# Optimization experiments

Measured on AMD Instinct MI355X. Metric: run time of the kernel, lower is better.

## Reference

```python
import jax, jax.numpy as jnp
import numpy as np

LN_EPS = 1e-5


def _layer_norm(x, w, b, eps=LN_EPS):
    mu = jnp.mean(x, axis=-1, keepdims=True)
    var = jnp.var(x, axis=-1, keepdims=True)
    return (x - mu) * jax.lax.rsqrt(var + eps) * w + b


def setup_inputs() -> dict:
    key = jax.random.key(0)
    ks = jax.random.split(key, 6)
    H, I, B, S = 1024, 4096, 4, 2048
    return {
        "x": jax.random.normal(ks[0], (B, S, H), jnp.float32),
        "ln_weight": jnp.ones((H,), jnp.float32),
        "ln_bias": jnp.zeros((H,), jnp.float32),
        "i2h_weight": jax.random.normal(ks[1], (2 * I, H), jnp.float32) * 0.02,
        "i2h_bias": jax.random.normal(ks[2], (2 * I,), jnp.float32) * 0.02,
        "h2o_weight": jax.random.normal(ks[3], (H, I), jnp.float32) * 0.02,
        "h2o_bias": jax.random.normal(ks[4], (H,), jnp.float32) * 0.02,
        "post_ln_weight": jnp.ones((H,), jnp.float32),
        "post_ln_bias": jnp.zeros((H,), jnp.float32),
    }


def reference(x, ln_weight, ln_bias, i2h_weight, i2h_bias, h2o_weight, h2o_bias,
              post_ln_weight, post_ln_bias):
    B, S, H = x.shape
    x2 = x.reshape(-1, H)  # [N, H]
    x_ln = _layer_norm(x2, ln_weight, ln_bias)
    # i2h: [N, 2I]
    pre = jnp.einsum('nh,oh->no', x_ln, i2h_weight) + i2h_bias
    I = pre.shape[-1] // 2
    pre_gate, lin = pre[:, :I], pre[:, I:]
    # gated gelu (tanh-approx, matching gelu_fused)
    hid = jax.nn.gelu(pre_gate, approximate=True) * lin
    out = jnp.einsum('ni,oi->no', hid, h2o_weight) + h2o_bias
    out = _layer_norm(out, post_ln_weight, post_ln_bias)
    out = out + x2  # residual (dropout=0)
    return out.reshape(B, S, H)
```

## Files before the change

### kernel.cpp

```cpp
#include <hip/hip_runtime.h>
#include <stdint.h>

#define N_ROWS 8192
#define H_DIM  1024
#define I_DIM  4096

typedef unsigned short u16;
typedef __bf16 bf16x8 __attribute__((ext_vector_type(8)));
typedef float f32x4 __attribute__((ext_vector_type(4)));
typedef u16 u16x4 __attribute__((ext_vector_type(4)));

#define BAR()   asm volatile("s_barrier" ::: "memory")
#define VMW(n)  asm volatile("s_waitcnt vmcnt(" #n ")" ::: "memory")

__device__ __forceinline__ u16 f2bf(float f) {
    union { float f; uint32_t u; } v; v.f = f;
    uint32_t u = v.u;
    u += 0x7FFFu + ((u >> 16) & 1u);
    return (u16)(u >> 16);
}

__device__ __forceinline__ float bf2f(u16 h) {
    union { uint32_t u; float f; } v; v.u = ((uint32_t)h) << 16;
    return v.f;
}

__device__ __forceinline__ float gelu_tanh(float x) {
    float u = 0.7978845608028654f * (x + 0.044715f * x * x * x);
    u = fminf(fmaxf(u, -15.f), 15.f);
    float e = __expf(2.f * u);
    float t = (e - 1.f) / (e + 1.f);
    return 0.5f * x * (1.f + t);
}

__device__ __forceinline__ void load_lds16(const void* g, void* l) {
    auto gp = reinterpret_cast<const __attribute__((address_space(1))) uint32_t*>(
        reinterpret_cast<uintptr_t>(g));
    auto lp = reinterpret_cast<__attribute__((address_space(3))) uint32_t*>(
        static_cast<uint32_t>(reinterpret_cast<uintptr_t>(l)));
    __builtin_amdgcn_global_load_lds(gp, lp, 16, 0, 0);
}

__global__ __launch_bounds__(512, 2) void gemm1_gated(
    const u16* __restrict__ A, const u16* __restrict__ W,
    const float* __restrict__ bias, u16* __restrict__ hid)
{
    __shared__ u16 lds[3 * 16384];
    const int t = threadIdx.x;
    const int lane = t & 63, wid = t >> 6;
    const int wm = wid >> 2, wn = wid & 3;
    const int g = lane >> 4, r16 = lane & 15;

    const int brow = blockIdx.y * 256;
    const int bcol = blockIdx.x * 128;

    const int tr = t >> 2;
    const int swz8 = ((t & 3) ^ ((tr >> 1) & 3)) * 8;
    const u16* pA = A + (size_t)(brow + tr) * H_DIM + swz8;
    const int j0 = tr, j1 = tr + 128;
    const int c0 = bcol + ((j0 >> 6) << 5) + (j0 & 31);
    const int c1 = bcol + ((j1 >> 6) << 5) + (j1 & 31);
    const u16* pB0 = W + (size_t)(((j0 & 63) < 32) ? c0 : (I_DIM + c0)) * H_DIM + swz8;
    const u16* pB1 = W + (size_t)(((j1 & 63) < 32) ? c1 : (I_DIM + c1)) * H_DIM + swz8;
    const int dst = t * 8;

    const int sl  = (g ^ ((r16 >> 1) & 3)) * 8;
    const int rdA = (wm * 128 + r16) * 32 + sl;
    const int rdB = 8192 + (wn * 64 + r16) * 32 + sl;

    f32x4 acc[8][4] = {};

#define STG1(S, k0) do { \
    load_lds16(pA  + (k0),                       (S) + dst); \
    load_lds16(pA  + (size_t)128 * H_DIM + (k0), (S) + 4096 + dst); \
    load_lds16(pB0 + (k0),                       (S) + 8192 + dst); \
    load_lds16(pB1 + (k0),                       (S) + 12288 + dst); } while (0)

    STG1(lds, 0);
    STG1(lds + 16384, 32);
    VMW(4); BAR();

    const int NT = H_DIM / 32;
    int bc = 0;
#pragma unroll 1
    for (int kt = 0; kt < NT; ++kt) {
        const u16* L = lds + bc * 16384;
        const bool st = (kt + 2 < NT);
        if (st) {
            u16* S = lds + ((bc + 2 >= 3) ? (bc - 1) : (bc + 2)) * 16384;
            STG1(S, (kt + 2) * 32);
        }
        bf16x8 af[8], bf[4];
#pragma unroll
        for (int m = 0; m < 8; ++m) af[m] = *(const bf16x8*)(L + rdA + m * 512);
#pragma unroll
        for (int n = 0; n < 4; ++n) bf[n] = *(const bf16x8*)(L + rdB + n * 512);
        __builtin_amdgcn_s_setprio(1);
#pragma unroll
        for (int m = 0; m < 8; ++m)
#pragma unroll
            for (int n = 0; n < 4; ++n)
                acc[m][n] = __builtin_amdgcn_mfma_f32_16x16x32_bf16(af[m], bf[n], acc[m][n], 0, 0, 0);
        __builtin_amdgcn_s_setprio(0);
        if (st) { VMW(4); } else { VMW(0); }
        BAR();
        bc = (bc == 2) ? 0 : bc + 1;
    }
#undef STG1

#pragma unroll
    for (int n = 0; n < 2; ++n) {
        const int cg = bcol + wn * 32 + n * 16 + r16;
        const float bgv = bias[cg], blv = bias[I_DIM + cg];
#pragma unroll
        for (int m = 0; m < 8; ++m) {
            const int row = brow + wm * 128 + m * 16 + g * 4;
            u16* hp = hid + (size_t)row * I_DIM + cg;
#pragma unroll
            for (int r = 0; r < 4; ++r) {
                float gate = acc[m][n][r] + bgv;
                float lin  = acc[m][n + 2][r] + blv;
                hp[(size_t)r * I_DIM] = f2bf(gelu_tanh(gate) * lin);
            }
        }
    }
}

__global__ __launch_bounds__(256, 3) void gemm2_k(
    const u16* __restrict__ A, const u16* __restrict__ W,
    const float* __restrict__ bias, u16* __restrict__ opb)
{
    __shared__ u16 lds[3 * 8192];
    const int t = threadIdx.x;
    const int lane = t & 63, wid = t >> 6;
    const int wm = wid >> 1, wn = wid & 1;
    const int g = lane >> 4, r16 = lane & 15;

    const int brow = blockIdx.y * 128;
    const int bcol = blockIdx.x * 128;

    const int tr = t >> 2;
    const int swz8 = ((t & 3) ^ ((tr >> 1) & 3)) * 8;
    const u16* pA = A + (size_t)(brow + tr) * I_DIM + swz8;
    const u16* pB = W + (size_t)(bcol + tr) * I_DIM + swz8;
    const int dst = t * 8;

    const int sl  = (g ^ ((r16 >> 1) & 3)) * 8;
    const int rdA = (wm * 64 + r16) * 32 + sl;
    const int rdB = 4096 + (wn * 64 + r16) * 32 + sl;

    f32x4 acc[4][4] = {};

#define STG2(S, k0) do { \
    load_lds16(pA + (k0),                      (S) + dst); \
    load_lds16(pA + (size_t)64 * I_DIM + (k0), (S) + 2048 + dst); \
    load_lds16(pB + (k0),                      (S) + 4096 + dst); \
    load_lds16(pB + (size_t)64 * I_DIM + (k0), (S) + 6144 + dst); } while (0)

    STG2(lds, 0);
    STG2(lds + 8192, 32);
    VMW(4); BAR();

    const int NT = I_DIM / 32;
    int bc = 0;
#pragma unroll 1
    for (int kt = 0; kt < NT; ++kt) {
        const u16* L = lds + bc * 8192;
        if (kt + 2 < NT) {
            u16* S = lds + ((bc + 2 >= 3) ? (bc - 1) : (bc + 2)) * 8192;
            STG2(S, (kt + 2) * 32);
        }
        bf16x8 af[4], bf[4];
#pragma unroll
        for (int m = 0; m < 4; ++m) af[m] = *(const bf16x8*)(L + rdA + m * 512);
#pragma unroll
        for (int n = 0; n < 4; ++n) bf[n] = *(const bf16x8*)(L + rdB + n * 512);
        __builtin_amdgcn_s_setprio(1);
#pragma unroll
        for (int m = 0; m < 4; ++m)
#pragma unroll
            for (int n = 0; n < 4; ++n)
                acc[m][n] = __builtin_amdgcn_mfma_f32_16x16x32_bf16(af[m], bf[n], acc[m][n], 0, 0, 0);
        __builtin_amdgcn_s_setprio(0);
        if (kt + 2 < NT) { VMW(4); } else { VMW(0); }
        BAR();
        bc = (bc == 2) ? 0 : bc + 1;
    }
#undef STG2

#pragma unroll
    for (int n = 0; n < 4; ++n) {
        const int cg = bcol + wn * 64 + n * 16 + r16;
        const float bv = bias[cg];
#pragma unroll
        for (int m = 0; m < 4; ++m) {
            const int row = brow + wm * 64 + m * 16 + g * 4;
            u16* op = opb + (size_t)row * H_DIM + cg;
#pragma unroll
            for (int r = 0; r < 4; ++r)
                op[(size_t)r * H_DIM] = f2bf(acc[m][n][r] + bv);
        }
    }
}

__device__ __forceinline__ void block_mean_var(float s, float s2, float* red, int t,
                                               float& mu, float& var) {
#pragma unroll
    for (int off = 32; off > 0; off >>= 1) {
        s  += __shfl_down(s, off);
        s2 += __shfl_down(s2, off);
    }
    const int wid = t >> 6;
    if ((t & 63) == 0) { red[wid] = s; red[4 + wid] = s2; }
    __syncthreads();
    if (t == 0) {
        float a = red[0] + red[1] + red[2] + red[3];
        float b = red[4] + red[5] + red[6] + red[7];
        red[0] = a * (1.f / H_DIM);
        red[1] = b * (1.f / H_DIM);
    }
    __syncthreads();
    mu = red[0];
    var = red[1] - mu * mu;
}

__global__ __launch_bounds__(256) void prep(
    const float* __restrict__ x, const float* __restrict__ lnw,
    const float* __restrict__ lnb, u16* __restrict__ xln,
    const float* __restrict__ w1, u16* __restrict__ w1b,
    const float* __restrict__ w2, u16* __restrict__ w2b)
{
    __shared__ float red[8];
    const int bid = blockIdx.x, t = threadIdx.x;
    if (bid < N_ROWS) {
        const float4 v = reinterpret_cast<const float4*>(x + (size_t)bid * H_DIM)[t];
        float mu, var;
        block_mean_var(v.x + v.y + v.z + v.w,
                       v.x * v.x + v.y * v.y + v.z * v.z + v.w * v.w, red, t, mu, var);
        const float rstd = rsqrtf(var + 1e-5f);
        const float4 wv = reinterpret_cast<const float4*>(lnw)[t];
        const float4 bv = reinterpret_cast<const float4*>(lnb)[t];
        u16x4 o;
        o.x = f2bf((v.x - mu) * rstd * wv.x + bv.x);
        o.y = f2bf((v.y - mu) * rstd * wv.y + bv.y);
        o.z = f2bf((v.z - mu) * rstd * wv.z + bv.z);
        o.w = f2bf((v.w - mu) * rstd * wv.w + bv.w);
        reinterpret_cast<u16x4*>(xln + (size_t)bid * H_DIM)[t] = o;
    } else if (bid < N_ROWS + 8192) {
        const int i = (bid - N_ROWS) * 256 + t;
        const float4 v = reinterpret_cast<const float4*>(w1)[i];
        u16x4 o = { f2bf(v.x), f2bf(v.y), f2bf(v.z), f2bf(v.w) };
        reinterpret_cast<u16x4*>(w1b)[i] = o;
    } else {
        const int i = (bid - N_ROWS - 8192) * 256 + t;
        const float4 v = reinterpret_cast<const float4*>(w2)[i];
        u16x4 o = { f2bf(v.x), f2bf(v.y), f2bf(v.z), f2bf(v.w) };
        reinterpret_cast<u16x4*>(w2b)[i] = o;
    }
}

__global__ void ln_post_res(const u16* __restrict__ op, const float* __restrict__ w,
                            const float* __restrict__ b, const float* __restrict__ x,
                            float* __restrict__ out)
{
    __shared__ float red[8];
    const int row = blockIdx.x, t = threadIdx.x;
    const u16x4 hv = reinterpret_cast<const u16x4*>(op + (size_t)row * H_DIM)[t];
    float4 v;
    v.x = bf2f(hv.x); v.y = bf2f(hv.y); v.z = bf2f(hv.z); v.w = bf2f(hv.w);
    float mu, var;
    block_mean_var(v.x + v.y + v.z + v.w,
                   v.x * v.x + v.y * v.y + v.z * v.z + v.w * v.w, red, t, mu, var);
    const float rstd = rsqrtf(var + 1e-5f);
    const float4 wv = reinterpret_cast<const float4*>(w)[t];
    const float4 bv = reinterpret_cast<const float4*>(b)[t];
    const float4 xv = reinterpret_cast<const float4*>(x + (size_t)row * H_DIM)[t];
    float4 o;
    o.x = (v.x - mu) * rstd * wv.x + bv.x + xv.x;
    o.y = (v.y - mu) * rstd * wv.y + bv.y + xv.y;
    o.z = (v.z - mu) * rstd * wv.z + bv.z + xv.z;
    o.w = (v.w - mu) * rstd * wv.w + bv.w + xv.w;
    reinterpret_cast<float4*>(out + (size_t)row * H_DIM)[t] = o;
}

extern "C" void kernel_launch(void* const* d_in, const int* in_sizes, int n_in,
                              void* d_out, int out_size, void* d_ws, size_t ws_size,
                              hipStream_t stream)
{
    const float* x   = (const float*)d_in[0];
    const float* lnw = (const float*)d_in[1];
    const float* lnb = (const float*)d_in[2];
    const float* w1  = (const float*)d_in[3];
    const float* b1  = (const float*)d_in[4];
    const float* w2  = (const float*)d_in[5];
    const float* b2  = (const float*)d_in[6];
    const float* pw  = (const float*)d_in[7];
    const float* pb  = (const float*)d_in[8];
    float* out = (float*)d_out;

    char* ws = (char*)d_ws;
    u16* xln = (u16*)(ws);
    u16* w1b = (u16*)(ws + (16u << 20));
    u16* hid = (u16*)(ws + (32u << 20));
    u16* w2b = (u16*)(ws + (96u << 20));
    u16* opb = (u16*)(ws);

    prep<<<20480, 256, 0, stream>>>(x, lnw, lnb, xln, w1, w1b, w2, w2b);
    gemm1_gated<<<dim3(I_DIM / 128, N_ROWS / 256), 512, 0, stream>>>(xln, w1b, b1, hid);
    gemm2_k<<<dim3(H_DIM / 128, N_ROWS / 128), 256, 0, stream>>>(hid, w2b, b2, opb);
    ln_post_res<<<N_ROWS, 256, 0, stream>>>(opb, pw, pb, x, out);
}
```

Baseline: 274.9 us.

## Switch GEMMs to 32x32 MFMA with B operands loaded directly into registers

Both GEMM kernels move from 16x16x32 to 32x32x16 bf16 MFMA tiles. Each wave now loads its B (weight) fragments straight from global memory into registers, one k-step ahead, so only A is staged through LDS. The LDS swizzle changes to match the new read pattern. gemm2 grows to 256-row tiles with 512 threads. The goal is less LDS traffic and fewer LDS reads per MFMA, at the cost of uncoalesced per-wave global loads for B and higher register pressure.

Measured after the change: 416.7 us. 51.5% more time.

```diff
diff --git a/kernel.cpp b/kernel.cpp
--- a/kernel.cpp
+++ b/kernel.cpp
@@ -7,7 +7,7 @@
 
 typedef unsigned short u16;
 typedef __bf16 bf16x8 __attribute__((ext_vector_type(8)));
-typedef float f32x4 __attribute__((ext_vector_type(4)));
+typedef float f32x16 __attribute__((ext_vector_type(16)));
 typedef u16 u16x4 __attribute__((ext_vector_type(4)));
 
 #define BAR()   asm volatile("s_barrier" ::: "memory")
@@ -45,88 +45,99 @@
     const u16* __restrict__ A, const u16* __restrict__ W,
     const float* __restrict__ bias, u16* __restrict__ hid)
 {
-    __shared__ u16 lds[3 * 16384];
+    __shared__ u16 lds[3 * 8192];
     const int t = threadIdx.x;
     const int lane = t & 63, wid = t >> 6;
     const int wm = wid >> 2, wn = wid & 3;
-    const int g = lane >> 4, r16 = lane & 15;
+    const int cl = lane & 31, kh = lane >> 5;
 
     const int brow = blockIdx.y * 256;
     const int bcol = blockIdx.x * 128;
 
     const int tr = t >> 2;
-    const int swz8 = ((t & 3) ^ ((tr >> 1) & 3)) * 8;
+    const int sstg = ((tr >> 1) & 3) ^ ((tr >> 3) & 3);
+    const int swz8 = ((t & 3) ^ sstg) * 8;
     const u16* pA = A + (size_t)(brow + tr) * H_DIM + swz8;
-    const int j0 = tr, j1 = tr + 128;
-    const int c0 = bcol + ((j0 >> 6) << 5) + (j0 & 31);
-    const int c1 = bcol + ((j1 >> 6) << 5) + (j1 & 31);
-    const u16* pB0 = W + (size_t)(((j0 & 63) < 32) ? c0 : (I_DIM + c0)) * H_DIM + swz8;
-    const u16* pB1 = W + (size_t)(((j1 & 63) < 32) ? c1 : (I_DIM + c1)) * H_DIM + swz8;
     const int dst = t * 8;
 
-    const int sl  = (g ^ ((r16 >> 1) & 3)) * 8;
-    const int rdA = (wm * 128 + r16) * 32 + sl;
-    const int rdB = 8192 + (wn * 64 + r16) * 32 + sl;
-
-    f32x4 acc[8][4] = {};
-
-#define STG1(S, k0) do { \
-    load_lds16(pA  + (k0),                       (S) + dst); \
-    load_lds16(pA  + (size_t)128 * H_DIM + (k0), (S) + 4096 + dst); \
-    load_lds16(pB0 + (k0),                       (S) + 8192 + dst); \
-    load_lds16(pB1 + (k0),                       (S) + 12288 + dst); } while (0)
-
-    STG1(lds, 0);
-    STG1(lds + 16384, 32);
+    const int s  = ((cl >> 1) & 3) ^ ((cl >> 3) & 3);
+    const int p0 = ((0 + kh) ^ s) * 8;
+    const int p1 = ((2 + kh) ^ s) * 8;
+    const int rdA = (wm * 128 + cl) * 32;
+
+    const u16* pBg = W + (size_t)(bcol + wn * 32 + cl) * H_DIM + kh * 8;
+    const u16* pBl = W + (size_t)(I_DIM + bcol + wn * 32 + cl) * H_DIM + kh * 8;
+
+    f32x16 acc[4][2] = {};
+
+#define G1_STAGE(k0, bs) do { \
+    u16* S = lds + (bs) * 8192; \
+    load_lds16(pA + (k0),                       S + dst); \
+    load_lds16(pA + (size_t)128 * H_DIM + (k0), S + 4096 + dst); } while (0)
+#define G1_LOADB(k0, B) do { \
+    B[0] = *(const bf16x8*)(pBg + (k0));        \
+    B[1] = *(const bf16x8*)(pBg + (k0) + 16);   \
+    B[2] = *(const bf16x8*)(pBl + (k0));        \
+    B[3] = *(const bf16x8*)(pBl + (k0) + 16);   } while (0)
+#define G1_COMP(bcur, B) do { \
+    const u16* L = lds + (bcur) * 8192 + rdA; \
+    __builtin_amdgcn_s_setprio(1); \
+    _Pragma("unroll") for (int ks = 0; ks < 2; ++ks) { \
+        const int pk = ks ? p1 : p0; \
+        _Pragma("unroll") for (int tm = 0; tm < 4; ++tm) { \
+            bf16x8 af = *(const bf16x8*)(L + tm * 1024 + pk); \
+            acc[tm][0] = __builtin_amdgcn_mfma_f32_32x32x16_bf16(af, B[ks],     acc[tm][0], 0, 0, 0); \
+            acc[tm][1] = __builtin_amdgcn_mfma_f32_32x32x16_bf16(af, B[2 + ks], acc[tm][1], 0, 0, 0); \
+        } } \
+    __builtin_amdgcn_s_setprio(0); } while (0)
+
+    bf16x8 b0[4], b1[4];
+    G1_STAGE(0, 0);
+    G1_STAGE(32, 1);
+    __builtin_amdgcn_sched_barrier(0);
+    G1_LOADB(0, b0);
     VMW(4); BAR();
 
-    const int NT = H_DIM / 32;
     int bc = 0;
 #pragma unroll 1
-    for (int kt = 0; kt < NT; ++kt) {
-        const u16* L = lds + bc * 16384;
-        const bool st = (kt + 2 < NT);
-        if (st) {
-            u16* S = lds + ((bc + 2 >= 3) ? (bc - 1) : (bc + 2)) * 16384;
-            STG1(S, (kt + 2) * 32);
-        }
-        bf16x8 af[8], bf[4];
-#pragma unroll
-        for (int m = 0; m < 8; ++m) af[m] = *(const bf16x8*)(L + rdA + m * 512);
-#pragma unroll
-        for (int n = 0; n < 4; ++n) bf[n] = *(const bf16x8*)(L + rdB + n * 512);
-        __builtin_amdgcn_s_setprio(1);
-#pragma unroll
-        for (int m = 0; m < 8; ++m)
-#pragma unroll
-            for (int n = 0; n < 4; ++n)
-                acc[m][n] = __builtin_amdgcn_mfma_f32_16x16x32_bf16(af[m], bf[n], acc[m][n], 0, 0, 0);
-        __builtin_amdgcn_s_setprio(0);
-        if (st) { VMW(4); } else { VMW(0); }
+    for (int i = 0; i < 16; ++i) {
+        const bool w = (i < 15);
+        if (w) G1_STAGE((2 * i + 2) * 32, (bc + 2 >= 3) ? bc - 1 : bc + 2);
+        __builtin_amdgcn_sched_barrier(0);
+        G1_LOADB((2 * i + 1) * 32, b1);
+        G1_COMP(bc, b0);
+        if (w) { VMW(6); }
         BAR();
         bc = (bc == 2) ? 0 : bc + 1;
-    }
-#undef STG1
-
-#pragma unroll
-    for (int n = 0; n < 2; ++n) {
-        const int cg = bcol + wn * 32 + n * 16 + r16;
-        const float bgv = bias[cg], blv = bias[I_DIM + cg];
-#pragma unroll
-        for (int m = 0; m < 8; ++m) {
-            const int row = brow + wm * 128 + m * 16 + g * 4;
-            u16* hp = hid + (size_t)row * I_DIM + cg;
-#pragma unroll
-            for (int r = 0; r < 4; ++r) {
-                float gate = acc[m][n][r] + bgv;
-                float lin  = acc[m][n + 2][r] + blv;
-                hp[(size_t)r * I_DIM] = f2bf(gelu_tanh(gate) * lin);
-            }
+        if (w) {
+            G1_STAGE((2 * i + 3) * 32, (bc + 2 >= 3) ? bc - 1 : bc + 2);
+            __builtin_amdgcn_sched_barrier(0);
+            G1_LOADB((2 * i + 2) * 32, b0);
         }
-    }
-}
-
-__global__ __launch_bounds__(256, 3) void gemm2_k(
+        G1_COMP(bc, b1);
+        if (w) { VMW(6); BAR(); }
+        bc = (bc == 2) ? 0 : bc + 1;
+    }
+#undef G1_STAGE
+#undef G1_LOADB
+#undef G1_COMP
+
+    const int colg = bcol + wn * 32 + cl;
+    const float bgv = bias[colg], blv = bias[I_DIM + colg];
+#pragma unroll
+    for (int tm = 0; tm < 4; ++tm) {
+        const int rowb = brow + wm * 128 + tm * 32 + 4 * kh;
+#pragma unroll
+        for (int r = 0; r < 16; ++r) {
+            const int row = rowb + (r & 3) + 8 * (r >> 2);
+            float gate = acc[tm][0][r] + bgv;
+            float lin  = acc[tm][1][r] + blv;
+            hid[(size_t)row * I_DIM + colg] = f2bf(gelu_tanh(gate) * lin);
+        }
+    }
+}
+
+__global__ __launch_bounds__(512, 2) void gemm2_k(
     const u16* __restrict__ A, const u16* __restrict__ W,
     const float* __restrict__ bias, u16* __restrict__ opb)
 {
@@ -134,71 +145,91 @@
     const int t = threadIdx.x;
     const int lane = t & 63, wid = t >> 6;
     const int wm = wid >> 1, wn = wid & 1;
-    const int g = lane >> 4, r16 = lane & 15;
-
-    const int brow = blockIdx.y * 128;
+    const int cl = lane & 31, kh = lane >> 5;
+
+    const int brow = blockIdx.y * 256;
     const int bcol = blockIdx.x * 128;
 
     const int tr = t >> 2;
-    const int swz8 = ((t & 3) ^ ((tr >> 1) & 3)) * 8;
+    const int sstg = ((tr >> 1) & 3) ^ ((tr >> 3) & 3);
+    const int swz8 = ((t & 3) ^ sstg) * 8;
     const u16* pA = A + (size_t)(brow + tr) * I_DIM + swz8;
-    const u16* pB = W + (size_t)(bcol + tr) * I_DIM + swz8;
     const int dst = t * 8;
 
-    const int sl  = (g ^ ((r16 >> 1) & 3)) * 8;
-    const int rdA = (wm * 64 + r16) * 32 + sl;
-    const int rdB = 4096 + (wn * 64 + r16) * 32 + sl;
-
-    f32x4 acc[4][4] = {};
-
-#define STG2(S, k0) do { \
-    load_lds16(pA + (k0),                      (S) + dst); \
-    load_lds16(pA + (size_t)64 * I_DIM + (k0), (S) + 2048 + dst); \
-    load_lds16(pB + (k0),                      (S) + 4096 + dst); \
-    load_lds16(pB + (size_t)64 * I_DIM + (k0), (S) + 6144 + dst); } while (0)
-
-    STG2(lds, 0);
-    STG2(lds + 8192, 32);
+    const int s  = ((cl >> 1) & 3) ^ ((cl >> 3) & 3);
+    const int p0 = ((0 + kh) ^ s) * 8;
+    const int p1 = ((2 + kh) ^ s) * 8;
+    const int rdA = (wm * 64 + cl) * 32;
+
+    const u16* pB0 = W + (size_t)(bcol + wn * 64 + cl) * I_DIM + kh * 8;
+    const u16* pB1 = W + (size_t)(bcol + wn * 64 + 32 + cl) * I_DIM + kh * 8;
+
+    f32x16 acc[2][2] = {};
+
+#define G2_STAGE(k0, bs) do { \
+    u16* S = lds + (bs) * 8192; \
+    load_lds16(pA + (k0),                       S + dst); \
+    load_lds16(pA + (size_t)128 * I_DIM + (k0), S + 4096 + dst); } while (0)
+#define G2_LOADB(k0, B) do { \
+    B[0] = *(const bf16x8*)(pB0 + (k0));        \
+    B[1] = *(const bf16x8*)(pB0 + (k0) + 16);   \
+    B[2] = *(const bf16x8*)(pB1 + (k0));        \
+    B[3] = *(const bf16x8*)(pB1 + (k0) + 16);   } while (0)
+#define G2_COMP(bcur, B) do { \
+    const u16* L = lds + (bcur) * 8192 + rdA; \
+    __builtin_amdgcn_s_setprio(1); \
+    _Pragma("unroll") for (int ks = 0; ks < 2; ++ks) { \
+        const int pk = ks ? p1 : p0; \
+        _Pragma("unroll") for (int tm = 0; tm < 2; ++tm) { \
+            bf16x8 af = *(const bf16x8*)(L + tm * 1024 + pk); \
+            acc[tm][0] = __builtin_amdgcn_mfma_f32_32x32x16_bf16(af, B[ks],     acc[tm][0], 0, 0, 0); \
+            acc[tm][1] = __builtin_amdgcn_mfma_f32_32x32x16_bf16(af, B[2 + ks], acc[tm][1], 0, 0, 0); \
+        } } \
+    __builtin_amdgcn_s_setprio(0); } while (0)
+
+    bf16x8 b0[4], b1[4];
+    G2_STAGE(0, 0);
+    G2_STAGE(32, 1);
+    __builtin_amdgcn_sched_barrier(0);
+    G2_LOADB(0, b0);
     VMW(4); BAR();
 
-    const int NT = I_DIM / 32;
     int bc = 0;
 #pragma unroll 1
-    for (int kt = 0; kt < NT; ++kt) {
-        const u16* L = lds + bc * 8192;
-        if (kt + 2 < NT) {
-            u16* S = lds + ((bc + 2 >= 3) ? (bc - 1) : (bc + 2)) * 8192;
-            STG2(S, (kt + 2) * 32);
-        }
-        bf16x8 af[4], bf[4];
-#pragma unroll
-        for (int m = 0; m < 4; ++m) af[m] = *(const bf16x8*)(L + rdA + m * 512);
-#pragma unroll
-        for (int n = 0; n < 4; ++n) bf[n] = *(const bf16x8*)(L + rdB + n * 512);
-        __builtin_amdgcn_s_setprio(1);
-#pragma unroll
-        for (int m = 0; m < 4; ++m)
-#pragma unroll
-            for (int n = 0; n < 4; ++n)
-                acc[m][n] = __builtin_amdgcn_mfma_f32_16x16x32_bf16(af[m], bf[n], acc[m][n], 0, 0, 0);
-        __builtin_amdgcn_s_setprio(0);
-        if (kt + 2 < NT) { VMW(4); } else { VMW(0); }
+    for (int i = 0; i < 64; ++i) {
+        const bool w = (i < 63);
+        if (w) G2_STAGE((2 * i + 2) * 32, (bc + 2 >= 3) ? bc - 1 : bc + 2);
+        __builtin_amdgcn_sched_barrier(0);
+        G2_LOADB((2 * i + 1) * 32, b1);
+        G2_COMP(bc, b0);
+        if (w) { VMW(6); }
         BAR();
         bc = (bc == 2) ? 0 : bc + 1;
-    }
-#undef STG2
-
-#pragma unroll
-    for (int n = 0; n < 4; ++n) {
-        const int cg = bcol + wn * 64 + n * 16 + r16;
-        const float bv = bias[cg];
-#pragma unroll
-        for (int m = 0; m < 4; ++m) {
-            const int row = brow + wm * 64 + m * 16 + g * 4;
-            u16* op = opb + (size_t)row * H_DIM + cg;
-#pragma unroll
-            for (int r = 0; r < 4; ++r)
-                op[(size_t)r * H_DIM] = f2bf(acc[m][n][r] + bv);
+        if (w) {
+            G2_STAGE((2 * i + 3) * 32, (bc + 2 >= 3) ? bc - 1 : bc + 2);
+            __builtin_amdgcn_sched_barrier(0);
+            G2_LOADB((2 * i + 2) * 32, b0);
+        }
+        G2_COMP(bc, b1);
+        if (w) { VMW(6); BAR(); }
+        bc = (bc == 2) ? 0 : bc + 1;
+    }
+#undef G2_STAGE
+#undef G2_LOADB
+#undef G2_COMP
+
+#pragma unroll
+    for (int tn = 0; tn < 2; ++tn) {
+        const int col = bcol + wn * 64 + tn * 32 + cl;
+        const float bv = bias[col];
+#pragma unroll
+        for (int tm = 0; tm < 2; ++tm) {
+            const int rowb = brow + wm * 64 + tm * 32 + 4 * kh;
+#pragma unroll
+            for (int r = 0; r < 16; ++r) {
+                const int row = rowb + (r & 3) + 8 * (r >> 2);
+                opb[(size_t)row * H_DIM + col] = f2bf(acc[tm][tn][r] + bv);
+            }
         }
     }
 }
@@ -307,6 +338,6 @@
 
     prep<<<20480, 256, 0, stream>>>(x, lnw, lnb, xln, w1, w1b, w2, w2b);
     gemm1_gated<<<dim3(I_DIM / 128, N_ROWS / 256), 512, 0, stream>>>(xln, w1b, b1, hid);
-    gemm2_k<<<dim3(H_DIM / 128, N_ROWS / 128), 256, 0, stream>>>(hid, w2b, b2, opb);
+    gemm2_k<<<dim3(H_DIM / 128, N_ROWS / 256), 512, 0, stream>>>(hid, w2b, b2, opb);
     ln_post_res<<<N_ROWS, 256, 0, stream>>>(opb, pw, pb, x, out);
 }
```
